# Optimization experiments

Hardware: AMD Instinct MI355X
Metric: run time of the kernel (lower is better)

The kernel has to match this reference:

```python
import jax, jax.numpy as jnp
import numpy as np

N_VERTS = 40962   # icosphere level-6 vertices
N_POOL = 10242    # icosphere level-5 vertices (post-pool)
K = 7             # 6 neighbors + self
C1, C2, C3 = 64, 64, 128
IN_CH, OUT_CH = 8, 64
BATCH = 8


def setup_inputs() -> dict:
    key = jax.random.key(0)
    ks = jax.random.split(key, 10)
    x = jax.random.normal(ks[0], (BATCH, IN_CH, N_VERTS), dtype=jnp.float32)
    # neighbor order: 6 random neighbors + self at every 7th slot (as in my_get_neighs_order)
    neb6 = jax.random.randint(ks[1], (N_VERTS, 6), 0, N_VERTS)
    nebs = jnp.concatenate([neb6, jnp.arange(N_VERTS)[:, None]], axis=1).reshape(-1).astype(jnp.int64)
    s1 = 1.0 / np.sqrt(IN_CH)
    s2 = 1.0 / np.sqrt(C1 * K)
    s3 = 1.0 / np.sqrt(C2)
    sf = 1.0 / np.sqrt(C3 * N_POOL)
    W1 = jax.random.uniform(ks[2], (C1, IN_CH), jnp.float32, -s1, s1)
    b1 = jax.random.uniform(ks[3], (C1,), jnp.float32, -s1, s1)
    W2 = jax.random.uniform(ks[4], (C2, C1, K), jnp.float32, -s2, s2)
    b2 = jax.random.uniform(ks[5], (C2,), jnp.float32, -s2, s2)
    W3 = jax.random.uniform(ks[6], (C3, C2), jnp.float32, -s3, s3)
    b3 = jax.random.uniform(ks[7], (C3,), jnp.float32, -s3, s3)
    Wfc = jax.random.uniform(ks[8], (OUT_CH, C3 * N_POOL), jnp.float32, -sf, sf)
    bfc = jax.random.uniform(ks[9], (OUT_CH,), jnp.float32, -sf, sf)
    return {"x": x, "nebs": nebs, "W1": W1, "b1": b1, "W2": W2, "b2": b2,
            "W3": W3, "b3": b3, "Wfc": Wfc, "bfc": bfc}


def reference(x, nebs, W1, b1, W2, b2, W3, b3, Wfc, bfc):
    B = x.shape[0]
    # conv1: 1x1 conv == pointwise matmul over channels
    h1 = jax.nn.relu(jnp.einsum('bci,oc->boi', x, W1) + b1[None, :, None])  # [B,64,N]
    # gather neighbor features, then stride-7 conv collapses the 7 neighbor slots
    g1 = h1[:, :, nebs].reshape(B, C1, N_VERTS, K)                           # [B,64,N,7]
    h2 = jax.nn.relu(jnp.einsum('bcnk,ock->bon', g1, W2) + b2[None, :, None])  # [B,64,N]
    # gather for the first 10242 vertices, maxpool over the 7 neighbor slots
    g2 = h2[:, :, nebs[:N_POOL * K]].reshape(B, C2, N_POOL, K)
    p = jnp.max(g2, axis=-1)                                                  # [B,64,10242]
    # conv3: 1x1 conv
    h3 = jax.nn.relu(jnp.einsum('bci,oc->boi', p, W3) + b3[None, :, None])   # [B,128,10242]
    # dropout is identity in eval mode
    flat = h3.reshape(B, -1)                                                  # [B, 128*10242]
    return flat @ Wfc.T + bfc                                                 # [B, out_ch]
```

## Files before the change

### kernel.cpp

```cpp
#include <hip/hip_runtime.h>

#define NV 40962
#define NP 10242
#define KNB 7
#define C1 64
#define C2 64
#define C3 128
#define INC 8
#define OC 64
#define B 8
#define FCK (C3*NP)
#define NCHUNK (FCK/128)
#define FBLK 1024

typedef __attribute__((ext_vector_type(8))) __bf16 bf16x8;
typedef __attribute__((ext_vector_type(4))) float f32x4;
typedef unsigned short ushort_t;
typedef unsigned int uint_t;

static __device__ __forceinline__ ushort_t f2bf(float f) {
    uint_t u = __float_as_uint(f);
    u = (u + 0x7FFFu + ((u >> 16) & 1u)) >> 16;
    return (ushort_t)u;
}
static __device__ __forceinline__ uint_t pack2(float a, float b) {
    return (uint_t)f2bf(a) | ((uint_t)f2bf(b) << 16);
}

__global__ __launch_bounds__(256) void k_pre(const float* __restrict__ x,
        const float* __restrict__ W1, const float* __restrict__ b1,
        ushort_t* __restrict__ h1bf, const float* __restrict__ W2,
        const float* __restrict__ W3, ushort_t* __restrict__ wsw) {
    __shared__ float sW[C1*INC];
    __shared__ float sb[C1];
    int tid = threadIdx.x;
    if (blockIdx.x >= 1281) {
        int idx = (blockIdx.x - 1281)*256 + tid;
        if (idx < 28672) {
            int j = idx & 7, lane = (idx >> 3) & 63, rest = idx >> 9;
            int ntile = rest & 3, kstep = rest >> 2;
            int quad = lane >> 4, col = lane & 15;
            int k = kstep*32 + quad*8 + j;
            int o = ntile*16 + col;
            int c = k & 63, knb = k >> 6;
            wsw[idx] = f2bf(W2[(size_t)o*(C1*KNB) + c*KNB + knb]);
        } else if (idx < 28672 + 8192) {
            int s = idx - 28672;
            int j = s & 7, lane = (s >> 3) & 63, rest = s >> 9;
            int ntile = rest & 7, kstep = rest >> 3;
            int quad = lane >> 4, col = lane & 15;
            int c = kstep*32 + quad*8 + j;
            int o3 = ntile*16 + col;
            wsw[idx] = f2bf(W3[(size_t)o3*C2 + c]);
        }
        return;
    }
    for (int i = tid; i < C1*INC; i += 256) sW[i] = W1[i];
    if (tid < C1) sb[tid] = b1[tid];
    __syncthreads();
    long g = (long)blockIdx.x*256 + tid;
    if (g >= (long)NV*B) return;
    int n = (int)(g >> 3);
    int b = (int)(g & 7);
    float xv[INC];
#pragma unroll
    for (int c = 0; c < INC; ++c) xv[c] = x[(size_t)b*INC*NV + (size_t)c*NV + n];
    uint4* outp = (uint4*)(h1bf + ((size_t)n*B + b)*C1);
#pragma unroll
    for (int og = 0; og < 8; ++og) {
        float h[8];
#pragma unroll
        for (int j = 0; j < 8; ++j) {
            int o = og*8 + j;
            float a = sb[o];
#pragma unroll
            for (int c = 0; c < INC; ++c) a += xv[c]*sW[o*INC + c];
            h[j] = fmaxf(a, 0.f);
        }
        uint4 u;
        u.x = pack2(h[0], h[1]); u.y = pack2(h[2], h[3]);
        u.z = pack2(h[4], h[5]); u.w = pack2(h[6], h[7]);
        outp[og] = u;
    }
}

__global__ __launch_bounds__(256) void k_conv2m(const ushort_t* __restrict__ h1bf,
        const int* __restrict__ nebs, const ushort_t* __restrict__ wsw,
        const float* __restrict__ b2, ushort_t* __restrict__ h2bf) {
    int tid = threadIdx.x;
    int wave = tid >> 6, lane = tid & 63;
    int quad = lane >> 4, col = lane & 15;
    int bsub = col & 7;
    int mblock = blockIdx.x * 128;
    int mbase[2];
    int rowt[2][KNB];
    f32x4 acc[2][4];
#pragma unroll
    for (int t = 0; t < 2; ++t) {
        mbase[t] = mblock + wave*32 + t*16;
        int v = (mbase[t] + col) >> 3;
        int vc = v < NV ? v : 0;
#pragma unroll
        for (int kn = 0; kn < KNB; ++kn) rowt[t][kn] = nebs[(size_t)vc*KNB + kn];
#pragma unroll
        for (int nt = 0; nt < 4; ++nt) acc[t][nt] = (f32x4){0.f, 0.f, 0.f, 0.f};
    }
    float bv[4];
#pragma unroll
    for (int nt = 0; nt < 4; ++nt) bv[nt] = b2[nt*16 + col];
    const bf16x8* W = (const bf16x8*)wsw;
#pragma unroll
    for (int ks = 0; ks < 14; ++ks) {
        int knb = ks >> 1;
        int c0 = (ks & 1)*32 + quad*8;
        bf16x8 a0 = *(const bf16x8*)(h1bf + ((size_t)rowt[0][knb]*B + bsub)*C1 + c0);
        bf16x8 a1 = *(const bf16x8*)(h1bf + ((size_t)rowt[1][knb]*B + bsub)*C1 + c0);
#pragma unroll
        for (int nt = 0; nt < 4; ++nt) {
            bf16x8 bf = W[(ks*4 + nt)*64 + lane];
            acc[0][nt] = __builtin_amdgcn_mfma_f32_16x16x32_bf16(a0, bf, acc[0][nt], 0, 0, 0);
            acc[1][nt] = __builtin_amdgcn_mfma_f32_16x16x32_bf16(a1, bf, acc[1][nt], 0, 0, 0);
        }
    }
#pragma unroll
    for (int t = 0; t < 2; ++t) {
#pragma unroll
        for (int r = 0; r < 4; ++r) {
            int m = mbase[t] + quad*4 + r;
            if ((m >> 3) < NV) {
#pragma unroll
                for (int nt = 0; nt < 4; ++nt) {
                    float val = fmaxf(acc[t][nt][r] + bv[nt], 0.f);
                    h2bf[(size_t)m*C2 + nt*16 + col] = f2bf(val);
                }
            }
        }
    }
}

__global__ __launch_bounds__(256) void k_poolconv3(const ushort_t* __restrict__ h2bf,
        const int* __restrict__ nebs, const ushort_t* __restrict__ wsw3,
        const float* __restrict__ b3, float* __restrict__ h3) {
    int tid = threadIdx.x;
    int wave = tid >> 6, lane = tid & 63;
    int quad = lane >> 4, col = lane & 15;
    int m0 = blockIdx.x*64 + wave*16;
    int m = m0 + col;
    int mc = ((m >> 3) < NP) ? m : 0;
    int v = mc >> 3, bsub = mc & 7;
    int rowt[KNB];
#pragma unroll
    for (int kn = 0; kn < KNB; ++kn) rowt[kn] = nebs[(size_t)v*KNB + kn];
    f32x4 acc[8];
#pragma unroll
    for (int nt = 0; nt < 8; ++nt) acc[nt] = (f32x4){0.f, 0.f, 0.f, 0.f};
    float bv[8];
#pragma unroll
    for (int nt = 0; nt < 8; ++nt) bv[nt] = b3[nt*16 + col];
    const bf16x8* W = (const bf16x8*)wsw3;
#pragma unroll
    for (int ks = 0; ks < 2; ++ks) {
        float mx[8];
#pragma unroll
        for (int i = 0; i < 8; ++i) mx[i] = -1e30f;
#pragma unroll
        for (int kn = 0; kn < KNB; ++kn) {
            uint4 u = *(const uint4*)(h2bf + ((size_t)rowt[kn]*B + bsub)*C2 + ks*32 + quad*8);
            uint_t ws[4] = {u.x, u.y, u.z, u.w};
#pragma unroll
            for (int i = 0; i < 4; ++i) {
                float lo = __uint_as_float((ws[i] & 0xFFFFu) << 16);
                float hi = __uint_as_float(ws[i] & 0xFFFF0000u);
                mx[2*i]   = fmaxf(mx[2*i], lo);
                mx[2*i+1] = fmaxf(mx[2*i+1], hi);
            }
        }
        uint4 pk;
        pk.x = (__float_as_uint(mx[0]) >> 16) | (__float_as_uint(mx[1]) & 0xFFFF0000u);
        pk.y = (__float_as_uint(mx[2]) >> 16) | (__float_as_uint(mx[3]) & 0xFFFF0000u);
        pk.z = (__float_as_uint(mx[4]) >> 16) | (__float_as_uint(mx[5]) & 0xFFFF0000u);
        pk.w = (__float_as_uint(mx[6]) >> 16) | (__float_as_uint(mx[7]) & 0xFFFF0000u);
        bf16x8 a;
        __builtin_memcpy(&a, &pk, 16);
#pragma unroll
        for (int nt = 0; nt < 8; ++nt) {
            bf16x8 bf = W[(ks*8 + nt)*64 + lane];
            acc[nt] = __builtin_amdgcn_mfma_f32_16x16x32_bf16(a, bf, acc[nt], 0, 0, 0);
        }
    }
#pragma unroll
    for (int r = 0; r < 4; ++r) {
        int mm = m0 + quad*4 + r;
        int vv = mm >> 3, b = mm & 7;
        if (vv < NP) {
#pragma unroll
            for (int nt = 0; nt < 8; ++nt) {
                int o3 = nt*16 + col;
                h3[(size_t)b*FCK + (size_t)o3*NP + vv] = fmaxf(acc[nt][r] + bv[nt], 0.f);
            }
        }
    }
}

__global__ __launch_bounds__(256) void k_fc(const float* __restrict__ h3,
        const float* __restrict__ Wfc, float* __restrict__ partial) {
    __shared__ float sH[B][128];
    __shared__ float sW[OC][129];
    int tid = threadIdx.x;
    int o = tid & 63;
    int tb = tid >> 6;
    float acc0 = 0.f, acc1 = 0.f;
    for (int ch = blockIdx.x; ch < NCHUNK; ch += FBLK) {
        size_t i0 = (size_t)ch * 128;
        __syncthreads();
        {
            int bb = tid >> 5, i4 = tid & 31;
            float4 f = *(const float4*)(h3 + (size_t)bb*FCK + i0 + i4*4);
            sH[bb][i4*4+0] = f.x; sH[bb][i4*4+1] = f.y;
            sH[bb][i4*4+2] = f.z; sH[bb][i4*4+3] = f.w;
        }
#pragma unroll
        for (int j = 0; j < 8; ++j) {
            int idx = tid + j*256;
            int oo = idx >> 5, i4 = idx & 31;
            float4 f = *(const float4*)(Wfc + (size_t)oo*FCK + i0 + i4*4);
            sW[oo][i4*4+0] = f.x; sW[oo][i4*4+1] = f.y;
            sW[oo][i4*4+2] = f.z; sW[oo][i4*4+3] = f.w;
        }
        __syncthreads();
#pragma unroll 8
        for (int ii = 0; ii < 128; ++ii) {
            float w = sW[o][ii];
            acc0 += w * sH[2*tb][ii];
            acc1 += w * sH[2*tb+1][ii];
        }
    }
    partial[((size_t)blockIdx.x*B + 2*tb  )*OC + o] = acc0;
    partial[((size_t)blockIdx.x*B + 2*tb+1)*OC + o] = acc1;
}

__global__ __launch_bounds__(256) void k_fcred(const float* __restrict__ partial,
        const float* __restrict__ bfc, float* __restrict__ out) {
    __shared__ float red[4][64];
    int b = blockIdx.x;
    int o = threadIdx.x & 63, jg = threadIdx.x >> 6;
    float s = 0.f;
    for (int j = jg; j < FBLK; j += 4) s += partial[((size_t)j*B + b)*OC + o];
    red[jg][o] = s;
    __syncthreads();
    if (jg == 0) out[b*OC + o] = red[0][o] + red[1][o] + red[2][o] + red[3][o] + bfc[o];
}

extern "C" void kernel_launch(void* const* d_in, const int* in_sizes, int n_in,
                              void* d_out, int out_size, void* d_ws, size_t ws_size,
                              hipStream_t stream) {
    const float* x    = (const float*)d_in[0];
    const int*   nebs = (const int*)d_in[1];
    const float* W1   = (const float*)d_in[2];
    const float* b1   = (const float*)d_in[3];
    const float* W2   = (const float*)d_in[4];
    const float* b2   = (const float*)d_in[5];
    const float* W3   = (const float*)d_in[6];
    const float* b3   = (const float*)d_in[7];
    const float* Wfc  = (const float*)d_in[8];
    const float* bfc  = (const float*)d_in[9];
    float* out = (float*)d_out;

    char* ws = (char*)d_ws;
    ushort_t* h1bf = (ushort_t*)(ws);
    ushort_t* h2bf = (ushort_t*)(ws + 42000000);
    float*    h3   = (float*)(ws + 96000000);
    ushort_t* wsw  = (ushort_t*)(ws + 140000000);
    float*    part = (float*)(ws + 141000000);
    ushort_t* wsw3 = wsw + 28672;

    k_pre<<<1425, 256, 0, stream>>>(x, W1, b1, h1bf, W2, W3, wsw);
    k_conv2m<<<2561, 256, 0, stream>>>(h1bf, nebs, wsw, b2, h2bf);
    k_poolconv3<<<1281, 256, 0, stream>>>(h2bf, nebs, wsw3, b3, h3);
    k_fc<<<FBLK, 256, 0, stream>>>(h3, Wfc, part);
    k_fcred<<<B, 256, 0, stream>>>(part, bfc, out);
}
```

Measured before the change: 660.5 us.

## Enlarge per-wave M tiles in conv kernels and swizzle vectorized FC shared memory

k_conv2m now gives each wave four 16-row MFMA tiles instead of two, and k_poolconv3 gives each wave two tiles instead of one, so each weight fragment load feeds more MFMAs. Grid sizes are halved to match. k_fc switches its shared-memory staging to float4 entries with an XOR swizzle and reads weights and activations as vectors, so LDS traffic is wider and bank conflicts drop. The larger tiles raise register pressure and leave fewer blocks in flight.

```diff
diff --git a/kernel.cpp b/kernel.cpp
--- a/kernel.cpp
+++ b/kernel.cpp
@@ -91,13 +91,13 @@
     int wave = tid >> 6, lane = tid & 63;
     int quad = lane >> 4, col = lane & 15;
     int bsub = col & 7;
-    int mblock = blockIdx.x * 128;
-    int mbase[2];
-    int rowt[2][KNB];
-    f32x4 acc[2][4];
-#pragma unroll
-    for (int t = 0; t < 2; ++t) {
-        mbase[t] = mblock + wave*32 + t*16;
+    int mblock = blockIdx.x * 256;
+    int mbase[4];
+    int rowt[4][KNB];
+    f32x4 acc[4][4];
+#pragma unroll
+    for (int t = 0; t < 4; ++t) {
+        mbase[t] = mblock + wave*64 + t*16;
         int v = (mbase[t] + col) >> 3;
         int vc = v < NV ? v : 0;
 #pragma unroll
@@ -113,17 +113,20 @@
     for (int ks = 0; ks < 14; ++ks) {
         int knb = ks >> 1;
         int c0 = (ks & 1)*32 + quad*8;
-        bf16x8 a0 = *(const bf16x8*)(h1bf + ((size_t)rowt[0][knb]*B + bsub)*C1 + c0);
-        bf16x8 a1 = *(const bf16x8*)(h1bf + ((size_t)rowt[1][knb]*B + bsub)*C1 + c0);
+        bf16x8 a[4];
+#pragma unroll
+        for (int t = 0; t < 4; ++t)
+            a[t] = *(const bf16x8*)(h1bf + ((size_t)rowt[t][knb]*B + bsub)*C1 + c0);
 #pragma unroll
         for (int nt = 0; nt < 4; ++nt) {
             bf16x8 bf = W[(ks*4 + nt)*64 + lane];
-            acc[0][nt] = __builtin_amdgcn_mfma_f32_16x16x32_bf16(a0, bf, acc[0][nt], 0, 0, 0);
-            acc[1][nt] = __builtin_amdgcn_mfma_f32_16x16x32_bf16(a1, bf, acc[1][nt], 0, 0, 0);
-        }
-    }
-#pragma unroll
-    for (int t = 0; t < 2; ++t) {
+#pragma unroll
+            for (int t = 0; t < 4; ++t)
+                acc[t][nt] = __builtin_amdgcn_mfma_f32_16x16x32_bf16(a[t], bf, acc[t][nt], 0, 0, 0);
+        }
+    }
+#pragma unroll
+    for (int t = 0; t < 4; ++t) {
 #pragma unroll
         for (int r = 0; r < 4; ++r) {
             int m = mbase[t] + quad*4 + r;
@@ -144,59 +147,74 @@
     int tid = threadIdx.x;
     int wave = tid >> 6, lane = tid & 63;
     int quad = lane >> 4, col = lane & 15;
-    int m0 = blockIdx.x*64 + wave*16;
-    int m = m0 + col;
-    int mc = ((m >> 3) < NP) ? m : 0;
-    int v = mc >> 3, bsub = mc & 7;
-    int rowt[KNB];
-#pragma unroll
-    for (int kn = 0; kn < KNB; ++kn) rowt[kn] = nebs[(size_t)v*KNB + kn];
-    f32x4 acc[8];
-#pragma unroll
-    for (int nt = 0; nt < 8; ++nt) acc[nt] = (f32x4){0.f, 0.f, 0.f, 0.f};
+    int m0 = blockIdx.x*128 + wave*32;
+    int rowt[2][KNB];
+    int bsub[2];
+#pragma unroll
+    for (int t = 0; t < 2; ++t) {
+        int m = m0 + t*16 + col;
+        int mc = ((m >> 3) < NP) ? m : 0;
+        int v = mc >> 3;
+        bsub[t] = mc & 7;
+#pragma unroll
+        for (int kn = 0; kn < KNB; ++kn) rowt[t][kn] = nebs[(size_t)v*KNB + kn];
+    }
+    f32x4 acc[2][8];
+#pragma unroll
+    for (int t = 0; t < 2; ++t)
+#pragma unroll
+        for (int nt = 0; nt < 8; ++nt) acc[t][nt] = (f32x4){0.f, 0.f, 0.f, 0.f};
     float bv[8];
 #pragma unroll
     for (int nt = 0; nt < 8; ++nt) bv[nt] = b3[nt*16 + col];
     const bf16x8* W = (const bf16x8*)wsw3;
 #pragma unroll
     for (int ks = 0; ks < 2; ++ks) {
-        float mx[8];
-#pragma unroll
-        for (int i = 0; i < 8; ++i) mx[i] = -1e30f;
-#pragma unroll
-        for (int kn = 0; kn < KNB; ++kn) {
-            uint4 u = *(const uint4*)(h2bf + ((size_t)rowt[kn]*B + bsub)*C2 + ks*32 + quad*8);
-            uint_t ws[4] = {u.x, u.y, u.z, u.w};
-#pragma unroll
-            for (int i = 0; i < 4; ++i) {
-                float lo = __uint_as_float((ws[i] & 0xFFFFu) << 16);
-                float hi = __uint_as_float(ws[i] & 0xFFFF0000u);
-                mx[2*i]   = fmaxf(mx[2*i], lo);
-                mx[2*i+1] = fmaxf(mx[2*i+1], hi);
+        bf16x8 a[2];
+#pragma unroll
+        for (int t = 0; t < 2; ++t) {
+            float mx[8];
+#pragma unroll
+            for (int i = 0; i < 8; ++i) mx[i] = -1e30f;
+#pragma unroll
+            for (int kn = 0; kn < KNB; ++kn) {
+                uint4 u = *(const uint4*)(h2bf + ((size_t)rowt[t][kn]*B + bsub[t])*C2 + ks*32 + quad*8);
+                uint_t ws[4] = {u.x, u.y, u.z, u.w};
+#pragma unroll
+                for (int i = 0; i < 4; ++i) {
+                    float lo = __uint_as_float((ws[i] & 0xFFFFu) << 16);
+                    float hi = __uint_as_float(ws[i] & 0xFFFF0000u);
+                    mx[2*i]   = fmaxf(mx[2*i], lo);
+                    mx[2*i+1] = fmaxf(mx[2*i+1], hi);
+                }
             }
-        }
-        uint4 pk;
-        pk.x = (__float_as_uint(mx[0]) >> 16) | (__float_as_uint(mx[1]) & 0xFFFF0000u);
-        pk.y = (__float_as_uint(mx[2]) >> 16) | (__float_as_uint(mx[3]) & 0xFFFF0000u);
-        pk.z = (__float_as_uint(mx[4]) >> 16) | (__float_as_uint(mx[5]) & 0xFFFF0000u);
-        pk.w = (__float_as_uint(mx[6]) >> 16) | (__float_as_uint(mx[7]) & 0xFFFF0000u);
-        bf16x8 a;
-        __builtin_memcpy(&a, &pk, 16);
+            uint4 pk;
+            pk.x = (__float_as_uint(mx[0]) >> 16) | (__float_as_uint(mx[1]) & 0xFFFF0000u);
+            pk.y = (__float_as_uint(mx[2]) >> 16) | (__float_as_uint(mx[3]) & 0xFFFF0000u);
+            pk.z = (__float_as_uint(mx[4]) >> 16) | (__float_as_uint(mx[5]) & 0xFFFF0000u);
+            pk.w = (__float_as_uint(mx[6]) >> 16) | (__float_as_uint(mx[7]) & 0xFFFF0000u);
+            __builtin_memcpy(&a[t], &pk, 16);
+        }
 #pragma unroll
         for (int nt = 0; nt < 8; ++nt) {
             bf16x8 bf = W[(ks*8 + nt)*64 + lane];
-            acc[nt] = __builtin_amdgcn_mfma_f32_16x16x32_bf16(a, bf, acc[nt], 0, 0, 0);
-        }
-    }
-#pragma unroll
-    for (int r = 0; r < 4; ++r) {
-        int mm = m0 + quad*4 + r;
-        int vv = mm >> 3, b = mm & 7;
-        if (vv < NP) {
-#pragma unroll
-            for (int nt = 0; nt < 8; ++nt) {
-                int o3 = nt*16 + col;
-                h3[(size_t)b*FCK + (size_t)o3*NP + vv] = fmaxf(acc[nt][r] + bv[nt], 0.f);
+#pragma unroll
+            for (int t = 0; t < 2; ++t)
+                acc[t][nt] = __builtin_amdgcn_mfma_f32_16x16x32_bf16(a[t], bf, acc[t][nt], 0, 0, 0);
+        }
+    }
+#pragma unroll
+    for (int t = 0; t < 2; ++t) {
+#pragma unroll
+        for (int r = 0; r < 4; ++r) {
+            int mm = m0 + t*16 + quad*4 + r;
+            int vv = mm >> 3, b = mm & 7;
+            if (vv < NP) {
+#pragma unroll
+                for (int nt = 0; nt < 8; ++nt) {
+                    int o3 = nt*16 + col;
+                    h3[(size_t)b*FCK + (size_t)o3*NP + vv] = fmaxf(acc[t][nt][r] + bv[nt], 0.f);
+                }
             }
         }
     }
@@ -204,39 +222,37 @@
 
 __global__ __launch_bounds__(256) void k_fc(const float* __restrict__ h3,
         const float* __restrict__ Wfc, float* __restrict__ partial) {
-    __shared__ float sH[B][128];
-    __shared__ float sW[OC][129];
-    int tid = threadIdx.x;
-    int o = tid & 63;
-    int tb = tid >> 6;
+    __shared__ f32x4 sW4[OC][32];
+    __shared__ f32x4 sH4[B][32];
+    int tid = threadIdx.x;
+    int wave = tid >> 6, lane = tid & 63;
+    int o  = wave*16 + (lane & 15);
+    int bp = lane >> 4;
+    int b0 = 2*bp, b1 = 2*bp + 1;
     float acc0 = 0.f, acc1 = 0.f;
+    int sb_ = tid >> 5, si4 = tid & 31;
     for (int ch = blockIdx.x; ch < NCHUNK; ch += FBLK) {
         size_t i0 = (size_t)ch * 128;
         __syncthreads();
-        {
-            int bb = tid >> 5, i4 = tid & 31;
-            float4 f = *(const float4*)(h3 + (size_t)bb*FCK + i0 + i4*4);
-            sH[bb][i4*4+0] = f.x; sH[bb][i4*4+1] = f.y;
-            sH[bb][i4*4+2] = f.z; sH[bb][i4*4+3] = f.w;
-        }
+        sH4[sb_][si4 ^ sb_] = *(const f32x4*)(h3 + (size_t)sb_*FCK + i0 + si4*4);
 #pragma unroll
         for (int j = 0; j < 8; ++j) {
-            int idx = tid + j*256;
+            int idx = j*256 + tid;
             int oo = idx >> 5, i4 = idx & 31;
-            float4 f = *(const float4*)(Wfc + (size_t)oo*FCK + i0 + i4*4);
-            sW[oo][i4*4+0] = f.x; sW[oo][i4*4+1] = f.y;
-            sW[oo][i4*4+2] = f.z; sW[oo][i4*4+3] = f.w;
+            sW4[oo][i4 ^ (oo & 7)] = *(const f32x4*)(Wfc + (size_t)oo*FCK + i0 + i4*4);
         }
         __syncthreads();
-#pragma unroll 8
-        for (int ii = 0; ii < 128; ++ii) {
-            float w = sW[o][ii];
-            acc0 += w * sH[2*tb][ii];
-            acc1 += w * sH[2*tb+1][ii];
-        }
-    }
-    partial[((size_t)blockIdx.x*B + 2*tb  )*OC + o] = acc0;
-    partial[((size_t)blockIdx.x*B + 2*tb+1)*OC + o] = acc1;
+#pragma unroll
+        for (int i4 = 0; i4 < 32; ++i4) {
+            f32x4 wv = sW4[o][i4 ^ (o & 7)];
+            f32x4 h0 = sH4[b0][i4 ^ b0];
+            f32x4 h1 = sH4[b1][i4 ^ b1];
+            acc0 += wv.x*h0.x + wv.y*h0.y + wv.z*h0.z + wv.w*h0.w;
+            acc1 += wv.x*h1.x + wv.y*h1.y + wv.z*h1.z + wv.w*h1.w;
+        }
+    }
+    partial[((size_t)blockIdx.x*B + b0)*OC + o] = acc0;
+    partial[((size_t)blockIdx.x*B + b1)*OC + o] = acc1;
 }
 
 __global__ __launch_bounds__(256) void k_fcred(const float* __restrict__ partial,
@@ -275,8 +291,8 @@
     ushort_t* wsw3 = wsw + 28672;
 
     k_pre<<<1425, 256, 0, stream>>>(x, W1, b1, h1bf, W2, W3, wsw);
-    k_conv2m<<<2561, 256, 0, stream>>>(h1bf, nebs, wsw, b2, h2bf);
-    k_poolconv3<<<1281, 256, 0, stream>>>(h2bf, nebs, wsw3, b3, h3);
+    k_conv2m<<<1281, 256, 0, stream>>>(h1bf, nebs, wsw, b2, h2bf);
+    k_poolconv3<<<641, 256, 0, stream>>>(h2bf, nebs, wsw3, b3, h3);
     k_fc<<<FBLK, 256, 0, stream>>>(h3, Wfc, part);
     k_fcred<<<B, 256, 0, stream>>>(part, bfc, out);
 }
```

Result: slower. 694.6 us (+5.2%).
